# Kernel optimization log

Measured on AMD Instinct MI355X. Metric: run time of the kernel, lower is better.

Reference implementation:

```python
import jax, jax.numpy as jnp
import numpy as np

ALPHA = 0.3

def setup_inputs() -> dict:
    key = jax.random.key(0)
    k1, k2, k3, k4 = jax.random.split(key, 4)
    bz, sl, n_pos = 64, 1024, 50
    a_arc = jax.random.normal(k1, (bz, sl, sl), dtype=jnp.float32)
    s_arc = jax.random.normal(k2, (bz, sl, sl), dtype=jnp.float32)
    adds = jax.random.randint(k3, (bz, sl), 0, n_pos, dtype=jnp.int32)
    pos = jax.random.randint(k4, (bz, sl), 0, n_pos, dtype=jnp.int32)
    return {"a_arc": a_arc, "s_arc": s_arc, "adds": adds, "pos": pos, "n_pos": n_pos}


def reference(a_arc, s_arc, adds, pos, n_pos):
    # Bin index for every (head, dep) pair: bin = adds[b,i]*n_pos + adds[b,j]
    bins_add = adds[:, :, None] * n_pos + adds[:, None, :]          # [bz, sl, sl] int32
    # Histogram: sum a_arc values per POS-pair bin (replaces the O(n_pos^2) masked loop)
    score_arc = jax.ops.segment_sum(
        a_arc.reshape(-1), bins_add.reshape(-1), num_segments=n_pos * n_pos)
    score_arc = jax.nn.sigmoid(score_arc)                            # [n_pos^2]
    # Broadcast the binned scores back onto s_arc via the pos-pair bins
    bins_pos = pos[:, :, None] * n_pos + pos[:, None, :]             # [bz, sl, sl]
    return s_arc + ALPHA * score_arc[bins_pos]
```

## Files before the change

kernel.cpp:

```cpp
#include <hip/hip_runtime.h>

constexpr int NPOS  = 50;
constexpr int NBINS = NPOS * NPOS;
constexpr int SL    = 1024;
constexpr int BZ    = 64;
constexpr float ALPHA = 0.3f;

constexpr int H_THREADS = 128;
constexpr int H_COLS    = 2 * H_THREADS;
constexpr int COLCHUNKS = SL / H_COLS;
constexpr int ROWSPLITS = 2;
constexpr int H_ROWS    = SL / ROWSPLITS;
constexpr int H_BLOCKS  = BZ * COLCHUNKS * ROWSPLITS;

constexpr int A_THREADS       = 256;
constexpr int ROWS_PER_BLOCK  = 32;
constexpr int BLOCKS_PER_B    = SL / ROWS_PER_BLOCK;
constexpr int A_BLOCKS        = BZ * BLOCKS_PER_B;

__global__ __launch_bounds__(H_THREADS) void hist_kernel(
    const float* __restrict__ a, const int* __restrict__ adds,
    float* __restrict__ g_hist) {
  __shared__ float accA[NPOS][H_THREADS];
  __shared__ float accB[NPOS][H_THREADS];
  __shared__ int   adds_s[SL];
  __shared__ int   cnt2[NPOS];
  __shared__ int   off2s[NPOS];
  __shared__ int   off2m[NPOS];
  __shared__ int   order2[H_COLS];

  const int tid    = threadIdx.x;
  const int b      = blockIdx.x / (COLCHUNKS * ROWSPLITS);
  const int rem    = blockIdx.x % (COLCHUNKS * ROWSPLITS);
  const int cc     = rem / ROWSPLITS;
  const int rsplit = rem % ROWSPLITS;
  const int i0     = rsplit * H_ROWS;

  {
    const int4* src = (const int4*)(adds + (size_t)b * SL);
    ((int4*)adds_s)[tid]             = src[tid];
    ((int4*)adds_s)[tid + H_THREADS] = src[tid + H_THREADS];
  }
  #pragma unroll
  for (int p = 0; p < NPOS; ++p) { accA[p][tid] = 0.0f; accB[p][tid] = 0.0f; }
  if (tid < NPOS) cnt2[tid] = 0;
  __syncthreads();

  const int j0 = cc * H_COLS + 2 * tid;
  const int q0 = adds_s[j0];
  const int q1 = adds_s[j0 + 1];

  const float2* __restrict__ P =
      (const float2*)(a + ((size_t)b * SL + i0) * SL + j0);
  constexpr int RSTRIDE = SL / 2;

  auto loadset = [&](float2 (&v)[16], int (&bs)[16], int R0) {
    #pragma unroll
    for (int k = 0; k < 16; ++k)
      v[k] = P[(size_t)(R0 + k) * RSTRIDE];
    #pragma unroll
    for (int k4 = 0; k4 < 4; ++k4) {
      const int4 b4 = *(const int4*)&adds_s[i0 + R0 + k4 * 4];
      bs[k4 * 4 + 0] = b4.x; bs[k4 * 4 + 1] = b4.y;
      bs[k4 * 4 + 2] = b4.z; bs[k4 * 4 + 3] = b4.w;
    }
  };
  auto rmwset = [&](float2 (&v)[16], int (&bs)[16]) {
    #pragma unroll
    for (int k = 0; k < 16; ++k) {
      accA[bs[k]][tid] += v[k].x;
      accB[bs[k]][tid] += v[k].y;
    }
  };

  float2 v0[16], v1[16];
  int    bs0[16], bs1[16];
  loadset(v0, bs0, 0);
  for (int r0 = 0; r0 < H_ROWS; r0 += 32) {
    loadset(v1, bs1, r0 + 16);
    rmwset(v0, bs0);
    if (r0 + 32 < H_ROWS) loadset(v0, bs0, r0 + 32);
    rmwset(v1, bs1);
  }

  atomicAdd(&cnt2[q0], 1);
  atomicAdd(&cnt2[q1], 1);
  __syncthreads();
  if (tid == 0) {
    int run = 0;
    for (int c = 0; c < NPOS; ++c) { off2s[c] = run; off2m[c] = run; run += cnt2[c]; }
  }
  __syncthreads();
  order2[atomicAdd(&off2m[q0], 1)] = 2 * tid;
  order2[atomicAdd(&off2m[q1], 1)] = 2 * tid + 1;
  __syncthreads();

  for (int bin = tid; bin < NBINS; bin += H_THREADS) {
    const int p  = bin / NPOS;
    const int qq = bin % NPOS;
    const int s0 = off2s[qq];
    const int n  = cnt2[qq];
    float s = 0.0f;
    for (int k = 0; k < n; ++k) {
      const int c = order2[s0 + k];
      s += (c & 1) ? accB[p][c >> 1] : accA[p][c >> 1];
    }
    atomicAdd(&g_hist[bin], s);
  }
}

__global__ __launch_bounds__(A_THREADS) void apply_kernel(
    const float* __restrict__ s, const int* __restrict__ pos,
    const float* __restrict__ g_hist, float* __restrict__ out) {
  __shared__ float sig[NBINS];
  __shared__ int   pos_s[SL];

  const int tid = threadIdx.x;
  const int b   = blockIdx.x / BLOCKS_PER_B;
  const int i0  = (blockIdx.x % BLOCKS_PER_B) * ROWS_PER_BLOCK;

  ((int4*)pos_s)[tid] = ((const int4*)(pos + (size_t)b * SL))[tid];
  for (int k = tid; k < NBINS; k += A_THREADS) {
    const float h = g_hist[k];
    sig[k] = 1.0f / (1.0f + __expf(-h));
  }
  __syncthreads();

  const int4 pj = ((const int4*)pos_s)[tid];
  const size_t rowoff = ((size_t)b * SL + i0) * SL;
  const float4* __restrict__ srow = (const float4*)(s + rowoff);
  float4* __restrict__ orow = (float4*)(out + rowoff);

  for (int r = 0; r < ROWS_PER_BLOCK; ++r) {
    const int base = pos_s[i0 + r] * NPOS;
    const float4 sv = srow[(size_t)r * (SL / 4) + tid];
    float4 ov;
    ov.x = sv.x + ALPHA * sig[base + pj.x];
    ov.y = sv.y + ALPHA * sig[base + pj.y];
    ov.z = sv.z + ALPHA * sig[base + pj.z];
    ov.w = sv.w + ALPHA * sig[base + pj.w];
    orow[(size_t)r * (SL / 4) + tid] = ov;
  }
}

extern "C" void kernel_launch(void* const* d_in, const int* in_sizes, int n_in,
                              void* d_out, int out_size, void* d_ws, size_t ws_size,
                              hipStream_t stream) {
  const float* a_arc = (const float*)d_in[0];
  const float* s_arc = (const float*)d_in[1];
  const int*   adds  = (const int*)d_in[2];
  const int*   pos   = (const int*)d_in[3];
  float* out    = (float*)d_out;
  float* g_hist = (float*)d_ws;

  hipMemsetAsync(g_hist, 0, NBINS * sizeof(float), stream);

  hist_kernel <<<H_BLOCKS, H_THREADS, 0, stream>>>(a_arc, adds, g_hist);
  apply_kernel<<<A_BLOCKS, A_THREADS, 0, stream>>>(s_arc, pos, g_hist, out);
}
```

Measured before the change: 190.2 us.

## Sort rows by bin and accumulate in registers instead of LDS read-modify-write

The histogram kernel now counting-sorts the rows of its slice by their adds bin. For each bin it sums that bin's rows in registers and writes the accumulator to shared memory once, instead of doing a shared-memory read-modify-write for every element. This removes roughly 1024 LDS RMW operations per thread. The cost is that global loads now follow a data-dependent row order, with small unrolled batches of 8 and less regular prefetching, which may reduce memory-level parallelism for very small bins.

```diff
diff --git a/kernel.cpp b/kernel.cpp
--- a/kernel.cpp
+++ b/kernel.cpp
@@ -24,9 +24,9 @@
   __shared__ float accA[NPOS][H_THREADS];
   __shared__ float accB[NPOS][H_THREADS];
   __shared__ int   adds_s[SL];
-  __shared__ int   cnt2[NPOS];
-  __shared__ int   off2s[NPOS];
-  __shared__ int   off2m[NPOS];
+  __shared__ int   orderR[H_ROWS];
+  __shared__ int   cntR[NPOS], offRs[NPOS], offRm[NPOS];
+  __shared__ int   cnt2[NPOS], off2s[NPOS], off2m[NPOS];
   __shared__ int   order2[H_COLS];
 
   const int tid    = threadIdx.x;
@@ -41,58 +41,59 @@
     ((int4*)adds_s)[tid]             = src[tid];
     ((int4*)adds_s)[tid + H_THREADS] = src[tid + H_THREADS];
   }
-  #pragma unroll
-  for (int p = 0; p < NPOS; ++p) { accA[p][tid] = 0.0f; accB[p][tid] = 0.0f; }
-  if (tid < NPOS) cnt2[tid] = 0;
+  if (tid < NPOS) { cntR[tid] = 0; cnt2[tid] = 0; }
   __syncthreads();
 
   const int j0 = cc * H_COLS + 2 * tid;
   const int q0 = adds_s[j0];
   const int q1 = adds_s[j0 + 1];
 
-  const float2* __restrict__ P =
-      (const float2*)(a + ((size_t)b * SL + i0) * SL + j0);
-  constexpr int RSTRIDE = SL / 2;
-
-  auto loadset = [&](float2 (&v)[16], int (&bs)[16], int R0) {
-    #pragma unroll
-    for (int k = 0; k < 16; ++k)
-      v[k] = P[(size_t)(R0 + k) * RSTRIDE];
-    #pragma unroll
-    for (int k4 = 0; k4 < 4; ++k4) {
-      const int4 b4 = *(const int4*)&adds_s[i0 + R0 + k4 * 4];
-      bs[k4 * 4 + 0] = b4.x; bs[k4 * 4 + 1] = b4.y;
-      bs[k4 * 4 + 2] = b4.z; bs[k4 * 4 + 3] = b4.w;
-    }
-  };
-  auto rmwset = [&](float2 (&v)[16], int (&bs)[16]) {
-    #pragma unroll
-    for (int k = 0; k < 16; ++k) {
-      accA[bs[k]][tid] += v[k].x;
-      accB[bs[k]][tid] += v[k].y;
-    }
-  };
-
-  float2 v0[16], v1[16];
-  int    bs0[16], bs1[16];
-  loadset(v0, bs0, 0);
-  for (int r0 = 0; r0 < H_ROWS; r0 += 32) {
-    loadset(v1, bs1, r0 + 16);
-    rmwset(v0, bs0);
-    if (r0 + 32 < H_ROWS) loadset(v0, bs0, r0 + 32);
-    rmwset(v1, bs1);
-  }
-
+  for (int r = tid; r < H_ROWS; r += H_THREADS)
+    atomicAdd(&cntR[adds_s[i0 + r]], 1);
   atomicAdd(&cnt2[q0], 1);
   atomicAdd(&cnt2[q1], 1);
   __syncthreads();
   if (tid == 0) {
     int run = 0;
+    for (int c = 0; c < NPOS; ++c) { offRs[c] = run; offRm[c] = run; run += cntR[c]; }
+  } else if (tid == 64) {
+    int run = 0;
     for (int c = 0; c < NPOS; ++c) { off2s[c] = run; off2m[c] = run; run += cnt2[c]; }
   }
   __syncthreads();
+  for (int r = tid; r < H_ROWS; r += H_THREADS)
+    orderR[atomicAdd(&offRm[adds_s[i0 + r]], 1)] = r;
   order2[atomicAdd(&off2m[q0], 1)] = 2 * tid;
   order2[atomicAdd(&off2m[q1], 1)] = 2 * tid + 1;
+  __syncthreads();
+
+  const float2* __restrict__ P =
+      (const float2*)(a + ((size_t)b * SL + i0) * SL + j0);
+  constexpr int RS = SL / 2;
+
+  for (int p = 0; p < NPOS; ++p) {
+    const int s0 = offRs[p];
+    const int n  = cntR[p];
+    float ax = 0.0f, ay = 0.0f;
+    int k = 0;
+    for (; k + 8 <= n; k += 8) {
+      int rr[8];
+      #pragma unroll
+      for (int u = 0; u < 8; ++u) rr[u] = orderR[s0 + k + u];
+      float2 vv[8];
+      #pragma unroll
+      for (int u = 0; u < 8; ++u) vv[u] = P[(size_t)rr[u] * RS];
+      #pragma unroll
+      for (int u = 0; u < 8; ++u) { ax += vv[u].x; ay += vv[u].y; }
+    }
+    for (; k < n; ++k) {
+      const int r = orderR[s0 + k];
+      const float2 v = P[(size_t)r * RS];
+      ax += v.x; ay += v.y;
+    }
+    accA[p][tid] = ax;
+    accB[p][tid] = ay;
+  }
   __syncthreads();
 
   for (int bin = tid; bin < NBINS; bin += H_THREADS) {
```

Measured after the change: 271.8 us. 1.43x slower.
